# Kernel tuning notes

Hardware: AMD Instinct MI355X
Metric: run time of the kernel (lower is better)

## Reference

```python
import jax, jax.numpy as jnp
import numpy as np

B, T, L, M = 64, 2000, 400, 80
SIGMA_FACTOR = 0.05
SIGMA_CAP = 10.0
SIGMA_MIN = 1.5
WARMUP_STEPS = 10000
GLOBAL_STEP = 0  # fresh loss module -> progress = 0
ENTROPY_TARGET = 3.5
ATTN_W_START = 1.0
ATTN_W_MIN = 0.2
EPS = 1e-8


def setup_inputs() -> dict:
    key = jax.random.key(0)
    ks = jax.random.split(key, 8)
    mel_out_postnet = jax.random.normal(ks[0], (B, T, M), jnp.float32)
    mel_out = jax.random.normal(ks[1], (B, T, M), jnp.float32)
    gate_out = jax.random.normal(ks[2], (B, T), jnp.float32)
    # alignments: stacked per-step attention, row-normalized like real softmax outputs
    a = jax.random.uniform(ks[3], (B, T, L), jnp.float32)
    alignments = a / jnp.sum(a, axis=-1, keepdims=True)
    mel_target = jax.random.normal(ks[4], (B, T, M), jnp.float32)
    gate_target = jnp.round(jax.random.uniform(ks[5], (B, T), jnp.float32))
    mel_lengths = jax.random.randint(ks[6], (B,), T // 2, T + 1, jnp.int32).at[0].set(T)
    text_lengths = jax.random.randint(ks[7], (B,), L // 2, L + 1, jnp.int32).at[0].set(L)
    return {
        "mel_out_postnet": mel_out_postnet, "mel_out": mel_out, "gate_out": gate_out,
        "alignments": alignments, "mel_target": mel_target, "gate_target": gate_target,
        "mel_lengths": mel_lengths, "text_lengths": text_lengths,
    }


def _diagonal_target(text_lengths):
    # sigma per batch element; global_step=0 -> progress=0 -> sigma = init_sigma
    init_sigma = jnp.clip(text_lengths.astype(jnp.float32) * SIGMA_FACTOR, 3.0, SIGMA_CAP)
    progress = min(1.0, GLOBAL_STEP / float(WARMUP_STEPS))
    sigma = init_sigma - (init_sigma - SIGMA_MIN) * progress  # [B]
    t = jnp.arange(T, dtype=jnp.int32)  # decoder steps
    Lb = text_lengths[:, None]  # [B,1]
    # expected_pos = min(int(t*Lb/T), Lb-1); positive ints -> integer floor div matches trunc
    exp_pos = jnp.minimum((t[None, :] * Lb) // T, Lb - 1).astype(jnp.float32)  # [B,T]
    pos = jnp.arange(L, dtype=jnp.float32)  # [L]
    z = (pos[None, None, :] - exp_pos[:, :, None]) / sigma[:, None, None]
    g = jnp.exp(-0.5 * z * z)  # [B,T,L]
    valid = (pos[None, None, :] < text_lengths[:, None, None].astype(jnp.float32))
    g = g * valid
    return g / (jnp.sum(g, axis=-1, keepdims=True) + EPS)


def reference(mel_out_postnet, mel_out, gate_out, alignments, mel_target,
              gate_target, mel_lengths, text_lengths):
    # masked L1 on mel (mel_target already [B,T,M], matching the torch transpose)
    valid = (jnp.arange(T)[None, :] < mel_lengths[:, None])[:, :, None]  # [B,T,1]
    vf = valid.astype(jnp.float32)
    n_valid = jnp.sum(vf) * M
    mel_loss_1 = jnp.sum(jnp.abs(mel_out - mel_target) * vf) / n_valid
    mel_loss_2 = jnp.sum(jnp.abs(mel_out_postnet - mel_target) * vf) / n_valid
    loss_mel = mel_loss_1 + mel_loss_2

    # BCEWithLogits, mean reduction (stable form)
    x, z_t = gate_out, gate_target
    loss_gate = jnp.mean(jnp.maximum(x, 0.0) - x * z_t + jnp.log1p(jnp.exp(-jnp.abs(x))))

    # guided-attention KL against diagonal Gaussian target
    target = _diagonal_target(text_lengths)  # [B,T,L]
    attn_safe = jnp.maximum(alignments, EPS)
    log_pred = jnp.log(attn_safe)
    kl_pw = jnp.where(target > 0.0, target * (jnp.log(jnp.maximum(target, EPS)) - log_pred), 0.0)
    attention_kl = jnp.sum(kl_pw) / B / T  # batchmean then / T_dec
    attention_kl = jnp.minimum(attention_kl, 150.0)

    # entropy-gated attention weight (python-float in torch -> stop_gradient)
    attn_entropy = jnp.mean(-jnp.sum(attn_safe * log_pred, axis=2))
    ratio = jnp.maximum(attn_entropy / ENTROPY_TARGET, 0.0)
    weight = jnp.where(attn_entropy <= ENTROPY_TARGET,
                       jnp.maximum(ATTN_W_MIN, ATTN_W_START * ratio),
                       ATTN_W_START)
    weight = jax.lax.stop_gradient(weight)

    total_loss = loss_mel + loss_gate + weight * attention_kl
    return (total_loss, loss_mel, loss_gate, attention_kl)
```

## Files before the change

kernel.cpp:

```cpp
#include <hip/hip_runtime.h>
#include <cstddef>
#include <cstdint>

#define B_ 64
#define T_ 2000
#define L_ 400
#define M_ 80
#define EPSF 1e-8f
#define LOG_EPSF -18.420680743952367f

#define NA 1024
#define NB 128
#define NC 2048

__device__ inline float waveReduce(float v) {
#pragma unroll
  for (int m = 32; m >= 1; m >>= 1) v += __shfl_xor(v, m, 64);
  return v;
}

__global__ __launch_bounds__(256) void mel_kernel(
    const float4* __restrict__ mo, const float4* __restrict__ mp,
    const float4* __restrict__ mt, const int* __restrict__ mel_lengths,
    double* __restrict__ partial) {
  const int N4 = B_ * T_ * M_ / 4;
  float acc = 0.f;
  const int stride = gridDim.x * blockDim.x;
  for (int i = blockIdx.x * blockDim.x + threadIdx.x; i < N4; i += stride) {
    int row = i / (M_ / 4);
    int b = row / T_;
    int t = row - b * T_;
    if (t < mel_lengths[b]) {
      float4 a = mo[i], c = mp[i], d = mt[i];
      acc += fabsf(a.x - d.x) + fabsf(a.y - d.y) + fabsf(a.z - d.z) + fabsf(a.w - d.w);
      acc += fabsf(c.x - d.x) + fabsf(c.y - d.y) + fabsf(c.z - d.z) + fabsf(c.w - d.w);
    }
  }
  float w = waveReduce(acc);
  __shared__ double sh[4];
  int lane = threadIdx.x & 63, wid = threadIdx.x >> 6;
  if (lane == 0) sh[wid] = (double)w;
  __syncthreads();
  if (threadIdx.x == 0) partial[blockIdx.x] = sh[0] + sh[1] + sh[2] + sh[3];
}

__global__ __launch_bounds__(256) void gate_kernel(
    const float* __restrict__ x, const float* __restrict__ zt,
    double* __restrict__ partial) {
  float acc = 0.f;
  const int stride = gridDim.x * blockDim.x;
  for (int i = blockIdx.x * blockDim.x + threadIdx.x; i < B_ * T_; i += stride) {
    float xv = x[i], z = zt[i];
    acc += fmaxf(xv, 0.f) - xv * z + log1pf(expf(-fabsf(xv)));
  }
  float w = waveReduce(acc);
  __shared__ double sh[4];
  int lane = threadIdx.x & 63, wid = threadIdx.x >> 6;
  if (lane == 0) sh[wid] = (double)w;
  __syncthreads();
  if (threadIdx.x == 0) partial[blockIdx.x] = sh[0] + sh[1] + sh[2] + sh[3];
}

__global__ __launch_bounds__(256) void attn_kernel(
    const float* __restrict__ align, const int* __restrict__ text_lengths,
    double* __restrict__ klP, double* __restrict__ entP) {
  const int lane = threadIdx.x & 63;
  const int wib = threadIdx.x >> 6;
  const int waveId = blockIdx.x * 4 + wib;
  const int numWaves = gridDim.x * 4;
  float kl_acc = 0.f, ent_acc = 0.f;
  for (int p = waveId; p < B_ * T_; p += numWaves) {
    int b = p / T_;
    int t = p - b * T_;
    int Lb = text_lengths[b];
    float sigma = fminf(fmaxf((float)Lb * 0.05f, 3.0f), 10.0f);
    float invsig = 1.0f / sigma;
    int epi = t * Lb / T_;
    int lim = Lb - 1;
    if (epi > lim) epi = lim;
    float ep = (float)epi;
    const float* row = align + (size_t)p * L_;
    float g[7], lp[7], ee[7];
    float S = 0.f;
#pragma unroll
    for (int k = 0; k < 7; ++k) {
      int l = lane + 64 * k;
      g[k] = 0.f; lp[k] = 0.f; ee[k] = 0.f;
      if (l < L_) {
        float a = row[l];
        float as = fmaxf(a, EPSF);
        float lpv = logf(as);
        lp[k] = lpv;
        ent_acc -= as * lpv;
        float z = ((float)l - ep) * invsig;
        float e = -0.5f * z * z;
        ee[k] = e;
        float gv = (l < Lb) ? expf(e) : 0.f;
        g[k] = gv;
        S += gv;
      }
    }
    S = waveReduce(S);
    float Se = S + EPSF;
    float inv = 1.0f / Se;
    float logSe = logf(Se);
#pragma unroll
    for (int k = 0; k < 7; ++k) {
      int l = lane + 64 * k;
      if (l < L_ && g[k] > 0.f) {
        float tgt = g[k] * inv;
        float lt = fmaxf(ee[k] - logSe, LOG_EPSF);
        kl_acc += tgt * (lt - lp[k]);
      }
    }
  }
  float klw = waveReduce(kl_acc);
  float entw = waveReduce(ent_acc);
  __shared__ double skl[4], sent[4];
  if (lane == 0) { skl[wib] = (double)klw; sent[wib] = (double)entw; }
  __syncthreads();
  if (threadIdx.x == 0) {
    klP[blockIdx.x] = skl[0] + skl[1] + skl[2] + skl[3];
    entP[blockIdx.x] = sent[0] + sent[1] + sent[2] + sent[3];
  }
}

__device__ double segSum(const double* __restrict__ p, int n, double* sh) {
  double a = 0.0;
  for (int i = threadIdx.x; i < n; i += 256) a += p[i];
  sh[threadIdx.x] = a;
  __syncthreads();
  for (int s = 128; s > 0; s >>= 1) {
    if ((int)threadIdx.x < s) sh[threadIdx.x] += sh[threadIdx.x + s];
    __syncthreads();
  }
  double r = sh[0];
  __syncthreads();
  return r;
}

__global__ __launch_bounds__(256) void finalize_kernel(
    const double* __restrict__ ws, const int* __restrict__ mel_lengths,
    float* __restrict__ out) {
  __shared__ double sh[256];
  double mel_sum  = segSum(ws, NA, sh);
  double gate_sum = segSum(ws + NA, NB, sh);
  double kl_sum   = segSum(ws + NA + NB, NC, sh);
  double ent_sum  = segSum(ws + NA + NB + NC, NC, sh);
  if (threadIdx.x == 0) {
    long nv = 0;
    for (int b = 0; b < B_; ++b) nv += mel_lengths[b];
    double n_valid = (double)nv * (double)M_;
    float loss_mel  = (float)(mel_sum / n_valid);
    float loss_gate = (float)(gate_sum / (double)(B_ * T_));
    float kl  = (float)(kl_sum / (double)(B_ * T_));
    kl = fminf(kl, 150.0f);
    float ent = (float)(ent_sum / (double)(B_ * T_));
    float ratio = fmaxf(ent / 3.5f, 0.0f);
    float weight = (ent <= 3.5f) ? fmaxf(0.2f, 1.0f * ratio) : 1.0f;
    out[0] = loss_mel + loss_gate + weight * kl;
    out[1] = loss_mel;
    out[2] = loss_gate;
    out[3] = kl;
  }
}

extern "C" void kernel_launch(void* const* d_in, const int* in_sizes, int n_in,
                              void* d_out, int out_size, void* d_ws, size_t ws_size,
                              hipStream_t stream) {
  const float* mel_out_postnet = (const float*)d_in[0];
  const float* mel_out         = (const float*)d_in[1];
  const float* gate_out        = (const float*)d_in[2];
  const float* alignments     = (const float*)d_in[3];
  const float* mel_target      = (const float*)d_in[4];
  const float* gate_target     = (const float*)d_in[5];
  const int*   mel_lengths     = (const int*)d_in[6];
  const int*   text_lengths    = (const int*)d_in[7];
  float* out = (float*)d_out;
  double* ws = (double*)d_ws;

  double* melP  = ws;
  double* gateP = ws + NA;
  double* klP   = ws + NA + NB;
  double* entP  = ws + NA + NB + NC;

  mel_kernel<<<dim3(NA), dim3(256), 0, stream>>>(
      (const float4*)mel_out, (const float4*)mel_out_postnet,
      (const float4*)mel_target, mel_lengths, melP);
  gate_kernel<<<dim3(NB), dim3(256), 0, stream>>>(gate_out, gate_target, gateP);
  attn_kernel<<<dim3(NC), dim3(256), 0, stream>>>(alignments, text_lengths, klP, entP);
  finalize_kernel<<<dim3(1), dim3(256), 0, stream>>>(ws, mel_lengths, out);
}
```

Measured before the change: 395.1 us.

## Fuse mel, gate and attention reductions into one kernel with fast math

```diff
diff --git a/kernel.cpp b/kernel.cpp
--- a/kernel.cpp
+++ b/kernel.cpp
@@ -9,9 +9,7 @@
 #define EPSF 1e-8f
 #define LOG_EPSF -18.420680743952367f
 
-#define NA 1024
-#define NB 128
-#define NC 2048
+#define NBLK 2048
 
 __device__ inline float waveReduce(float v) {
 #pragma unroll
@@ -19,55 +17,38 @@
   return v;
 }
 
-__global__ __launch_bounds__(256) void mel_kernel(
+__global__ __launch_bounds__(256) void fused_kernel(
     const float4* __restrict__ mo, const float4* __restrict__ mp,
-    const float4* __restrict__ mt, const int* __restrict__ mel_lengths,
-    double* __restrict__ partial) {
-  const int N4 = B_ * T_ * M_ / 4;
-  float acc = 0.f;
-  const int stride = gridDim.x * blockDim.x;
-  for (int i = blockIdx.x * blockDim.x + threadIdx.x; i < N4; i += stride) {
+    const float4* __restrict__ mt, const float* __restrict__ gx,
+    const float* __restrict__ gz, const float* __restrict__ align,
+    const int* __restrict__ mel_lengths, const int* __restrict__ text_lengths,
+    double* __restrict__ ws) {
+  const int tid = blockIdx.x * 256 + threadIdx.x;
+  const int nthreads = NBLK * 256;
+
+  float mel_acc = 0.f;
+  const int N4 = B_ * T_ * (M_ / 4);
+  for (int i = tid; i < N4; i += nthreads) {
     int row = i / (M_ / 4);
     int b = row / T_;
     int t = row - b * T_;
     if (t < mel_lengths[b]) {
       float4 a = mo[i], c = mp[i], d = mt[i];
-      acc += fabsf(a.x - d.x) + fabsf(a.y - d.y) + fabsf(a.z - d.z) + fabsf(a.w - d.w);
-      acc += fabsf(c.x - d.x) + fabsf(c.y - d.y) + fabsf(c.z - d.z) + fabsf(c.w - d.w);
+      mel_acc += fabsf(a.x - d.x) + fabsf(a.y - d.y) + fabsf(a.z - d.z) + fabsf(a.w - d.w)
+               + fabsf(c.x - d.x) + fabsf(c.y - d.y) + fabsf(c.z - d.z) + fabsf(c.w - d.w);
     }
   }
-  float w = waveReduce(acc);
-  __shared__ double sh[4];
-  int lane = threadIdx.x & 63, wid = threadIdx.x >> 6;
-  if (lane == 0) sh[wid] = (double)w;
-  __syncthreads();
-  if (threadIdx.x == 0) partial[blockIdx.x] = sh[0] + sh[1] + sh[2] + sh[3];
-}
 
-__global__ __launch_bounds__(256) void gate_kernel(
-    const float* __restrict__ x, const float* __restrict__ zt,
-    double* __restrict__ partial) {
-  float acc = 0.f;
-  const int stride = gridDim.x * blockDim.x;
-  for (int i = blockIdx.x * blockDim.x + threadIdx.x; i < B_ * T_; i += stride) {
-    float xv = x[i], z = zt[i];
-    acc += fmaxf(xv, 0.f) - xv * z + log1pf(expf(-fabsf(xv)));
+  float gate_acc = 0.f;
+  for (int i = tid; i < B_ * T_; i += nthreads) {
+    float xv = gx[i], z = gz[i];
+    gate_acc += fmaxf(xv, 0.f) - xv * z + log1pf(__expf(-fabsf(xv)));
   }
-  float w = waveReduce(acc);
-  __shared__ double sh[4];
-  int lane = threadIdx.x & 63, wid = threadIdx.x >> 6;
-  if (lane == 0) sh[wid] = (double)w;
-  __syncthreads();
-  if (threadIdx.x == 0) partial[blockIdx.x] = sh[0] + sh[1] + sh[2] + sh[3];
-}
 
-__global__ __launch_bounds__(256) void attn_kernel(
-    const float* __restrict__ align, const int* __restrict__ text_lengths,
-    double* __restrict__ klP, double* __restrict__ entP) {
   const int lane = threadIdx.x & 63;
   const int wib = threadIdx.x >> 6;
   const int waveId = blockIdx.x * 4 + wib;
-  const int numWaves = gridDim.x * 4;
+  const int numWaves = NBLK * 4;
   float kl_acc = 0.f, ent_acc = 0.f;
   for (int p = waveId; p < B_ * T_; p += numWaves) {
     int b = p / T_;
@@ -89,13 +70,13 @@
       if (l < L_) {
         float a = row[l];
         float as = fmaxf(a, EPSF);
-        float lpv = logf(as);
+        float lpv = __logf(as);
         lp[k] = lpv;
         ent_acc -= as * lpv;
         float z = ((float)l - ep) * invsig;
         float e = -0.5f * z * z;
         ee[k] = e;
-        float gv = (l < Lb) ? expf(e) : 0.f;
+        float gv = (l < Lb) ? __expf(e) : 0.f;
         g[k] = gv;
         S += gv;
       }
@@ -103,7 +84,7 @@
     S = waveReduce(S);
     float Se = S + EPSF;
     float inv = 1.0f / Se;
-    float logSe = logf(Se);
+    float logSe = __logf(Se);
 #pragma unroll
     for (int k = 0; k < 7; ++k) {
       int l = lane + 64 * k;
@@ -114,14 +95,22 @@
       }
     }
   }
-  float klw = waveReduce(kl_acc);
-  float entw = waveReduce(ent_acc);
-  __shared__ double skl[4], sent[4];
-  if (lane == 0) { skl[wib] = (double)klw; sent[wib] = (double)entw; }
+
+  float w0 = waveReduce(mel_acc);
+  float w1 = waveReduce(gate_acc);
+  float w2 = waveReduce(kl_acc);
+  float w3 = waveReduce(ent_acc);
+  __shared__ double sh[4][4];
+  if (lane == 0) {
+    sh[wib][0] = (double)w0; sh[wib][1] = (double)w1;
+    sh[wib][2] = (double)w2; sh[wib][3] = (double)w3;
+  }
   __syncthreads();
   if (threadIdx.x == 0) {
-    klP[blockIdx.x] = skl[0] + skl[1] + skl[2] + skl[3];
-    entP[blockIdx.x] = sent[0] + sent[1] + sent[2] + sent[3];
+    ws[blockIdx.x]            = sh[0][0] + sh[1][0] + sh[2][0] + sh[3][0];
+    ws[NBLK + blockIdx.x]     = sh[0][1] + sh[1][1] + sh[2][1] + sh[3][1];
+    ws[2 * NBLK + blockIdx.x] = sh[0][2] + sh[1][2] + sh[2][2] + sh[3][2];
+    ws[3 * NBLK + blockIdx.x] = sh[0][3] + sh[1][3] + sh[2][3] + sh[3][3];
   }
 }
 
@@ -143,10 +132,10 @@
     const double* __restrict__ ws, const int* __restrict__ mel_lengths,
     float* __restrict__ out) {
   __shared__ double sh[256];
-  double mel_sum  = segSum(ws, NA, sh);
-  double gate_sum = segSum(ws + NA, NB, sh);
-  double kl_sum   = segSum(ws + NA + NB, NC, sh);
-  double ent_sum  = segSum(ws + NA + NB + NC, NC, sh);
+  double mel_sum  = segSum(ws, NBLK, sh);
+  double gate_sum = segSum(ws + NBLK, NBLK, sh);
+  double kl_sum   = segSum(ws + 2 * NBLK, NBLK, sh);
+  double ent_sum  = segSum(ws + 3 * NBLK, NBLK, sh);
   if (threadIdx.x == 0) {
     long nv = 0;
     for (int b = 0; b < B_; ++b) nv += mel_lengths[b];
@@ -171,7 +160,7 @@
   const float* mel_out_postnet = (const float*)d_in[0];
   const float* mel_out         = (const float*)d_in[1];
   const float* gate_out        = (const float*)d_in[2];
-  const float* alignments     = (const float*)d_in[3];
+  const float* alignments      = (const float*)d_in[3];
   const float* mel_target      = (const float*)d_in[4];
   const float* gate_target     = (const float*)d_in[5];
   const int*   mel_lengths     = (const int*)d_in[6];
@@ -179,15 +168,9 @@
   float* out = (float*)d_out;
   double* ws = (double*)d_ws;
 
-  double* melP  = ws;
-  double* gateP = ws + NA;
-  double* klP   = ws + NA + NB;
-  double* entP  = ws + NA + NB + NC;
-
-  mel_kernel<<<dim3(NA), dim3(256), 0, stream>>>(
+  fused_kernel<<<dim3(NBLK), dim3(256), 0, stream>>>(
       (const float4*)mel_out, (const float4*)mel_out_postnet,
-      (const float4*)mel_target, mel_lengths, melP);
-  gate_kernel<<<dim3(NB), dim3(256), 0, stream>>>(gate_out, gate_target, gateP);
-  attn_kernel<<<dim3(NC), dim3(256), 0, stream>>>(alignments, text_lengths, klP, entP);
+      (const float4*)mel_target, gate_out, gate_target,
+      alignments, mel_lengths, text_lengths, ws);
   finalize_kernel<<<dim3(1), dim3(256), 0, stream>>>(ws, mel_lengths, out);
 }
```

After: 389.9 us. Within noise of the previous version (-1.3%).
